# Optimization experiments

Measured on AMD Instinct MI355X. Metric: run time of the kernel, lower is better.

The kernel has to match this reference:

```python
import jax, jax.numpy as jnp
import numpy as np

B, L, D, H = 4, 1024, 1024, 16
HS = D // H
BLOCK = 1024
EPS = 1e-5


def setup_inputs() -> dict:
    key = jax.random.key(0)
    ks = jax.random.split(key, 12)
    s = 0.02
    return {
        "x": jax.random.normal(ks[0], (B, L, D), jnp.float32),
        "ln1_w": jnp.ones((D,), jnp.float32),
        "ln1_b": jnp.zeros((D,), jnp.float32),
        "Wqkv": jax.random.normal(ks[1], (D, 3 * D), jnp.float32) * s,
        "bqkv": jnp.zeros((3 * D,), jnp.float32),
        "Wproj": jax.random.normal(ks[2], (D, D), jnp.float32) * s,
        "bproj": jnp.zeros((D,), jnp.float32),
        "Er": jax.random.normal(ks[3], (BLOCK, HS), jnp.float32) * s,
        "ln2_w": jnp.ones((D,), jnp.float32),
        "ln2_b": jnp.zeros((D,), jnp.float32),
        "Wfc": jax.random.normal(ks[4], (D, 4 * D), jnp.float32) * s,
        "bfc": jnp.zeros((4 * D,), jnp.float32),
        "Wfc2": jax.random.normal(ks[5], (4 * D, D), jnp.float32) * s,
        "bfc2": jnp.zeros((D,), jnp.float32),
    }


def _layernorm(x, w, b):
    mu = jnp.mean(x, axis=-1, keepdims=True)
    var = jnp.mean(jnp.square(x - mu), axis=-1, keepdims=True)
    return (x - mu) * jax.lax.rsqrt(var + EPS) * w + b


def _skew(QEr):
    # Music-Transformer skew: pad one zero column on the left of last dim,
    # reshape (B,H,L,L+1) -> (B,H,L+1,L), drop first row.
    b, h, l, _ = QEr.shape
    padded = jnp.pad(QEr, ((0, 0), (0, 0), (0, 0), (1, 0)))
    return padded.reshape(b, h, l + 1, l)[:, :, 1:, :]


def _block(x, ln1_w, ln1_b, Wqkv, bqkv, Wproj, bproj, Er,
           ln2_w, ln2_b, Wfc, bfc, Wfc2, bfc2):
    b, l, d = x.shape
    # --- attention on ln_1(x) ---
    h = _layernorm(x, ln1_w, ln1_b)
    qkv = h @ Wqkv + bqkv                      # (B, L, 3D)
    q, k, v = jnp.split(qkv, 3, axis=-1)
    q = q.reshape(b, l, H, HS).transpose(0, 2, 1, 3)  # (B,H,L,hs)
    k = k.reshape(b, l, H, HS).transpose(0, 2, 1, 3)
    v = v.reshape(b, l, H, HS).transpose(0, 2, 1, 3)

    start = BLOCK - l
    Er_t = Er[start:, :].T                     # (hs, L)
    QEr = jnp.einsum('bhld,dm->bhlm', q, Er_t)  # (B,H,L,L)
    Srel = _skew(QEr)

    QKt = jnp.einsum('bhld,bhmd->bhlm', q, k)  # (B,H,L,L)
    scale = 1.0 / jnp.sqrt(jnp.asarray(HS, x.dtype))
    att = (QKt + Srel) * scale
    causal = jnp.tril(jnp.ones((l, l), bool))
    att = jnp.where(causal, att, jnp.asarray(-jnp.inf, att.dtype))
    att = jax.nn.softmax(att, axis=-1)
    y = jnp.einsum('bhlm,bhmd->bhld', att, v)  # (B,H,L,hs)
    y = y.transpose(0, 2, 1, 3).reshape(b, l, d)
    a = y @ Wproj + bproj

    x = x + a
    # --- MLP on ln_2(x) ---
    h2 = _layernorm(x, ln2_w, ln2_b)
    m = jax.nn.gelu(h2 @ Wfc + bfc, approximate=False) @ Wfc2 + bfc2
    return x + m


def reference(x, ln1_w, ln1_b, Wqkv, bqkv, Wproj, bproj, Er,
              ln2_w, ln2_b, Wfc, bfc, Wfc2, bfc2):
    return _block(x, ln1_w, ln1_b, Wqkv, bqkv, Wproj, bproj, Er,
                  ln2_w, ln2_b, Wfc, bfc, Wfc2, bfc2)
```

## Files before the change

kernel.cpp:

```cpp
#include <hip/hip_runtime.h>
#include <hip/hip_bf16.h>
#include <math.h>

typedef __attribute__((ext_vector_type(8))) __bf16 bf16x8;
typedef __attribute__((ext_vector_type(4))) float f32x4;

#define LL 1024
#define DD 1024
#define HH 16

#define GLOAD16(g, l)                                              \
  __builtin_amdgcn_global_load_lds(                                \
      (const __attribute__((address_space(1))) void*)(g),          \
      (__attribute__((address_space(3))) void*)(l), 16, 0, 0)

#define FENCE asm volatile("" ::: "memory")
#define BARRIER do { FENCE; __builtin_amdgcn_s_barrier(); FENCE; } while (0)
#define SCHEDB __builtin_amdgcn_sched_barrier(0)

__global__ __launch_bounds__(256) void transpose_cvt(const float* __restrict__ W,
                                                     __hip_bfloat16* __restrict__ Wt,
                                                     int R, int C) {
  __shared__ float tile[32][33];
  int tx = threadIdx.x;
  int r0 = blockIdx.y * 32, c0 = blockIdx.x * 32;
  int r = tx >> 3, c4 = (tx & 7) * 4;
  float4 v = *(const float4*)&W[(size_t)(r0 + r) * C + c0 + c4];
  tile[r][c4 + 0] = v.x; tile[r][c4 + 1] = v.y;
  tile[r][c4 + 2] = v.z; tile[r][c4 + 3] = v.w;
  __syncthreads();
  int c = tx >> 3, r4 = (tx & 7) * 4;
  __hip_bfloat16 o[4];
#pragma unroll
  for (int j = 0; j < 4; ++j) o[j] = __float2bfloat16(tile[r4 + j][c]);
  *(uint2*)&Wt[(size_t)(c0 + c) * R + r0 + r4] = *(const uint2*)o;
}

__global__ __launch_bounds__(256) void cvt_er(const float* __restrict__ Er,
                                              __hip_bfloat16* __restrict__ Erb) {
  int i = blockIdx.x * 256 + threadIdx.x;
  float4 v = *(const float4*)&Er[(size_t)i * 4];
  __hip_bfloat16 o[4];
  o[0] = __float2bfloat16(v.x); o[1] = __float2bfloat16(v.y);
  o[2] = __float2bfloat16(v.z); o[3] = __float2bfloat16(v.w);
  *(uint2*)&Erb[(size_t)i * 4] = *(const uint2*)o;
}

__global__ __launch_bounds__(256) void ln_kernel(const float* __restrict__ X,
                                                 const float* __restrict__ w,
                                                 const float* __restrict__ b,
                                                 __hip_bfloat16* __restrict__ out) {
  int row = blockIdx.x;
  int tid = threadIdx.x;
  const float* xr = X + (size_t)row * DD;
  float4 v = *(const float4*)&xr[tid * 4];
  float s = v.x + v.y + v.z + v.w;
  float s2 = v.x * v.x + v.y * v.y + v.z * v.z + v.w * v.w;
#pragma unroll
  for (int m = 1; m < 64; m <<= 1) {
    s += __shfl_xor(s, m);
    s2 += __shfl_xor(s2, m);
  }
  __shared__ float ps[4], ps2[4];
  int wv_ = tid >> 6, lane = tid & 63;
  if (lane == 0) { ps[wv_] = s; ps2[wv_] = s2; }
  __syncthreads();
  float ts = ps[0] + ps[1] + ps[2] + ps[3];
  float ts2 = ps2[0] + ps2[1] + ps2[2] + ps2[3];
  float mu = ts * (1.0f / DD);
  float var = ts2 * (1.0f / DD) - mu * mu;
  float rs = rsqrtf(var + 1e-5f);
  float4 wv = *(const float4*)&w[tid * 4];
  float4 bv = *(const float4*)&b[tid * 4];
  __hip_bfloat16 o[4];
  o[0] = __float2bfloat16((v.x - mu) * rs * wv.x + bv.x);
  o[1] = __float2bfloat16((v.y - mu) * rs * wv.y + bv.y);
  o[2] = __float2bfloat16((v.z - mu) * rs * wv.z + bv.z);
  o[3] = __float2bfloat16((v.w - mu) * rs * wv.w + bv.w);
  *(uint2*)&out[(size_t)row * DD + tid * 4] = *(const uint2*)o;
}

template <int EPI>
__global__ __launch_bounds__(512, 4) void gemm256x128(const __hip_bfloat16* __restrict__ A,
                                                      const __hip_bfloat16* __restrict__ Bt,
                                                      const float* __restrict__ bias,
                                                      const float* __restrict__ resid,
                                                      void* __restrict__ Cout,
                                                      int M, int N, int K) {
  __shared__ __hip_bfloat16 Ab[3][256][32];
  __shared__ __hip_bfloat16 Bb[3][128][32];
  const int tid = threadIdx.x, lane = tid & 63, w = tid >> 6;
  const int wm = w >> 1, wn = w & 1;

  int nbx = gridDim.x, nwg = nbx * gridDim.y;
  int orig = blockIdx.y * nbx + blockIdx.x;
  int cpx = nwg >> 3;
  int wgid = (orig & 7) * cpx + (orig >> 3);
  int bm0 = (wgid / nbx) * 256, bn0 = (wgid % nbx) * 128;

  const int fr = lane & 15, kq = lane >> 4;
  const int sg = ((lane & 3) ^ ((lane >> 3) & 3)) * 8;
  const int srw = lane >> 2;

  auto stageA = [&](int c, int g, int k0) {
    int u = w * 2 + g;
    const __hip_bfloat16* src = A + (size_t)(bm0 + u * 16 + srw) * K + k0 + sg;
    GLOAD16(src, (char*)Ab + c * 16384 + u * 1024);
  };
  auto stageB = [&](int c, int k0) {
    const __hip_bfloat16* src = Bt + (size_t)(bn0 + w * 16 + srw) * K + k0 + sg;
    GLOAD16(src, (char*)Bb + c * 8192 + w * 1024);
  };
  const int swz = ((kq ^ ((fr >> 1) & 3)) << 4);
  auto ldA = [&](int c, int r) -> bf16x8 {
    return *(const bf16x8*)((const char*)Ab + c * 16384 + r * 64 + swz);
  };
  auto ldB = [&](int c, int r) -> bf16x8 {
    return *(const bf16x8*)((const char*)Bb + c * 8192 + r * 64 + swz);
  };

  f32x4 acc[4][4] = {};
  bf16x8 a[4], b[4];

  const int nt = K >> 5;
#pragma unroll
  for (int tt = 0; tt < 2; ++tt) {
    stageA(tt, 0, tt * 32); stageA(tt, 1, tt * 32); stageB(tt, tt * 32);
  }
  asm volatile("s_waitcnt vmcnt(3)" ::: "memory");
  BARRIER;

  int cur = 0, nxt = 2;
  for (int t = 0; t < nt; ++t) {
#pragma unroll
    for (int mf = 0; mf < 4; ++mf) a[mf] = ldA(cur, wm * 64 + mf * 16 + fr);
#pragma unroll
    for (int nf = 0; nf < 4; ++nf) b[nf] = ldB(cur, wn * 64 + nf * 16 + fr);
    if (t + 2 < nt) {
      stageA(nxt, 0, (t + 2) * 32); stageA(nxt, 1, (t + 2) * 32); stageB(nxt, (t + 2) * 32);
    }
    __builtin_amdgcn_s_setprio(1);
#pragma unroll
    for (int mf = 0; mf < 4; ++mf)
#pragma unroll
      for (int nf = 0; nf < 4; ++nf)
        acc[mf][nf] = __builtin_amdgcn_mfma_f32_16x16x32_bf16(a[mf], b[nf], acc[mf][nf], 0, 0, 0);
    __builtin_amdgcn_s_setprio(0);
    if (t <= nt - 3)      { asm volatile("s_waitcnt vmcnt(3)" ::: "memory"); }
    else if (t == nt - 2) { asm volatile("s_waitcnt vmcnt(0)" ::: "memory"); }
    BARRIER;
    cur = (cur == 2) ? 0 : cur + 1;
    nxt = (nxt == 2) ? 0 : nxt + 1;
  }

#pragma unroll
  for (int nf = 0; nf < 4; ++nf) {
    int col = bn0 + wn * 64 + nf * 16 + fr;
    float bsv = bias[col];
#pragma unroll
    for (int mf = 0; mf < 4; ++mf) {
      int rowb = bm0 + wm * 64 + mf * 16 + kq * 4;
#pragma unroll
      for (int j = 0; j < 4; ++j) {
        int row = rowb + j;
        float v = acc[mf][nf][j] + bsv;
        if (EPI == 1) v = 0.5f * v * (1.0f + erff(v * 0.7071067811865476f));
        if (EPI == 2) {
          ((float*)Cout)[(size_t)row * N + col] = v + resid[(size_t)row * N + col];
        } else {
          ((__hip_bfloat16*)Cout)[(size_t)row * N + col] = __float2bfloat16(v);
        }
      }
    }
  }
}

template <int EPI>
__global__ __launch_bounds__(256) void gemm128p(const __hip_bfloat16* __restrict__ A,
                                                const __hip_bfloat16* __restrict__ Bt,
                                                const float* __restrict__ bias,
                                                const float* __restrict__ resid,
                                                void* __restrict__ Cout,
                                                int M, int N, int K) {
  __shared__ __hip_bfloat16 Ab[5][128][32];
  __shared__ __hip_bfloat16 Bb[5][128][32];
  const int tid = threadIdx.x, lane = tid & 63, w = tid >> 6;
  const int wm = w >> 1, wn = w & 1;

  int nbx = gridDim.x, nwg = nbx * gridDim.y;
  int orig = blockIdx.y * nbx + blockIdx.x;
  int cpx = nwg >> 3;
  int wgid = (orig & 7) * cpx + (orig >> 3);
  int bm0 = (wgid / nbx) * 128, bn0 = (wgid % nbx) * 128;

  const int fr = lane & 15, kq = lane >> 4;
  const int sg = ((lane & 3) ^ ((lane >> 3) & 3)) * 8;
  const int srw = lane >> 2;

  auto stageA = [&](int c, int half, int k0) {
    const __hip_bfloat16* src =
        A + (size_t)(bm0 + half * 64 + w * 16 + srw) * K + k0 + sg;
    GLOAD16(src, (char*)Ab + c * 8192 + half * 4096 + w * 1024);
  };
  auto stageB = [&](int c, int half, int k0) {
    const __hip_bfloat16* src =
        Bt + (size_t)(bn0 + half * 64 + w * 16 + srw) * K + k0 + sg;
    GLOAD16(src, (char*)Bb + c * 8192 + half * 4096 + w * 1024);
  };
  const int swz = ((kq ^ ((fr >> 1) & 3)) << 4);
  auto ldA = [&](int c, int r) -> bf16x8 {
    return *(const bf16x8*)((const char*)Ab + c * 8192 + r * 64 + swz);
  };
  auto ldB = [&](int c, int r) -> bf16x8 {
    return *(const bf16x8*)((const char*)Bb + c * 8192 + r * 64 + swz);
  };

  f32x4 acc[4][4] = {};
  bf16x8 a[4], b[4];

  const int nt = K >> 5;
#pragma unroll
  for (int tt = 0; tt < 4; ++tt) {
    stageA(tt, 0, tt * 32); stageA(tt, 1, tt * 32);
    stageB(tt, 0, tt * 32); stageB(tt, 1, tt * 32);
  }
  asm volatile("s_waitcnt vmcnt(12)" ::: "memory");
  BARRIER;

  int cur = 0, nxt = 4;
  for (int t = 0; t < nt; ++t) {
    const int kn = (t + 4) * 32;
    const bool st = (t + 4 < nt);
#pragma unroll
    for (int mf = 0; mf < 4; ++mf) a[mf] = ldA(cur, wm * 64 + mf * 16 + fr);
#pragma unroll
    for (int nf = 0; nf < 4; ++nf) b[nf] = ldB(cur, wn * 64 + nf * 16 + fr);
    if (st) {
      stageA(nxt, 0, kn); stageA(nxt, 1, kn);
      stageB(nxt, 0, kn); stageB(nxt, 1, kn);
    }
    BARRIER; SCHEDB;
    __builtin_amdgcn_s_setprio(1);
#pragma unroll
    for (int mf = 0; mf < 4; ++mf)
#pragma unroll
      for (int nf = 0; nf < 4; ++nf)
        acc[mf][nf] = __builtin_amdgcn_mfma_f32_16x16x32_bf16(a[mf], b[nf], acc[mf][nf], 0, 0, 0);
    __builtin_amdgcn_s_setprio(0);
    SCHEDB;
    if (t <= nt - 5)      { asm volatile("s_waitcnt vmcnt(12)" ::: "memory"); }
    else if (t == nt - 4) { asm volatile("s_waitcnt vmcnt(8)" ::: "memory"); }
    else if (t == nt - 3) { asm volatile("s_waitcnt vmcnt(4)" ::: "memory"); }
    else if (t == nt - 2) { asm volatile("s_waitcnt vmcnt(0)" ::: "memory"); }
    BARRIER;
    cur = (cur == 4) ? 0 : cur + 1;
    nxt = (nxt == 4) ? 0 : nxt + 1;
  }

#pragma unroll
  for (int nf = 0; nf < 4; ++nf) {
    int col = bn0 + wn * 64 + nf * 16 + fr;
    float bsv = bias[col];
#pragma unroll
    for (int mf = 0; mf < 4; ++mf) {
      int rowb = bm0 + wm * 64 + mf * 16 + kq * 4;
#pragma unroll
      for (int j = 0; j < 4; ++j) {
        int row = rowb + j;
        float v = acc[mf][nf][j] + bsv;
        if (EPI == 1) v = 0.5f * v * (1.0f + erff(v * 0.7071067811865476f));
        if (EPI == 2) {
          ((float*)Cout)[(size_t)row * N + col] = v + resid[(size_t)row * N + col];
        } else {
          ((__hip_bfloat16*)Cout)[(size_t)row * N + col] = __float2bfloat16(v);
        }
      }
    }
  }
}

__global__ __launch_bounds__(256) void attn_mfma(const __hip_bfloat16* __restrict__ qkv,
                                                 const __hip_bfloat16* __restrict__ Erb,
                                                 __hip_bfloat16* __restrict__ Y) {
  __shared__ __hip_bfloat16 k_s[64][72];
  __shared__ __hip_bfloat16 er_s[128][72];
  __shared__ __hip_bfloat16 p_s[4][16][72];
  __shared__ __hip_bfloat16 g_s[4][16][128];
  __shared__ __hip_bfloat16 vt_s[64 * 64];

  int bid = blockIdx.x;
  int qi = 15 - (bid >> 6);
  int head = bid & 63;
  int h = head & 15, b = head >> 4;
  int l0 = qi * 64;
  int tid = threadIdx.x, lane = tid & 63, w = tid >> 6;
  const int fr = lane & 15, kq = lane >> 4;

  const __hip_bfloat16* base = qkv + (size_t)b * (LL * 3072) + h * 64;

  bf16x8 qf[2];
  {
    const __hip_bfloat16* q0 = base + (size_t)(l0 + 16 * w + fr) * 3072 + kq * 8;
    qf[0] = *(const bf16x8*)q0;
    qf[1] = *(const bf16x8*)(q0 + 32);
  }

  const int ksr = tid >> 2, ksd = (tid & 3) * 16;
  const __hip_bfloat16* ksrc = base + 1024 + (size_t)ksr * 3072 + ksd;
  const int vc = (tid >> 3) * 2, vd0 = (tid & 7) * 8;
  const __hip_bfloat16* vsrc = base + 2048 + (size_t)vc * 3072 + vd0;
  const int e0r = tid >> 1, e0c = (tid & 1) * 32;
  const int err = tid >> 2, erc = (tid & 3) * 16;

  uint4 kst0, kst1, vst0, vst1;
  uint4 est0, est1, est2, est3;
  uint4 ers0, ers1;

  {
    kst0 = *(const uint4*)ksrc; kst1 = *(const uint4*)(ksrc + 8);
    vst0 = *(const uint4*)vsrc; vst1 = *(const uint4*)(vsrc + 3072);
    int m = min(max(960 - l0 + e0r, 0), 1023);
    const __hip_bfloat16* ep = Erb + (size_t)m * 64 + e0c;
    est0 = *(const uint4*)ep;        est1 = *(const uint4*)(ep + 8);
    est2 = *(const uint4*)(ep + 16); est3 = *(const uint4*)(ep + 24);
  }

  f32x4 oacc[4] = {};
  float m_run[4], s_run[4];
#pragma unroll
  for (int j = 0; j < 4; ++j) { m_run[j] = -1e30f; s_run[j] = 0.f; }

  auto gchunk = [&](int hf) {
#pragma unroll
    for (int g = 0; g < 4; ++g) {
      int cc = hf * 64 + 16 * g + fr, kc = kq * 8;
      bf16x8 e0 = *(const bf16x8*)&er_s[cc][kc];
      bf16x8 e1 = *(const bf16x8*)&er_s[cc][kc + 32];
      f32x4 gacc = {};
      gacc = __builtin_amdgcn_mfma_f32_16x16x32_bf16(qf[0], e0, gacc, 0, 0, 0);
      gacc = __builtin_amdgcn_mfma_f32_16x16x32_bf16(qf[1], e1, gacc, 0, 0, 0);
#pragma unroll
      for (int j = 0; j < 4; ++j)
        g_s[w][kq * 4 + j][hf * 64 + 16 * g + fr] = __float2bfloat16(gacc[j]);
    }
  };

  for (int t = 0; t <= qi; ++t) {
    __syncthreads();
    *(uint4*)&k_s[ksr][ksd] = kst0;
    *(uint4*)&k_s[ksr][ksd + 8] = kst1;
    {
      const uint16_t* h0 = (const uint16_t*)&vst0;
      const uint16_t* h1 = (const uint16_t*)&vst1;
#pragma unroll
      for (int j = 0; j < 8; ++j) {
        int d = vd0 + j;
        uint32_t pk = (uint32_t)h0[j] | ((uint32_t)h1[j] << 16);
        uint32_t byte = ((uint32_t)d << 7) + 2u * (uint32_t)vc;
        byte ^= (uint32_t)(((d & 7) ^ (d >> 3)) << 4);
        *(uint32_t*)((char*)vt_s + byte) = pk;
      }
    }
    if (t == 0) {
      *(uint4*)&er_s[e0r][e0c]      = est0;
      *(uint4*)&er_s[e0r][e0c + 8]  = est1;
      *(uint4*)&er_s[e0r][e0c + 16] = est2;
      *(uint4*)&er_s[e0r][e0c + 24] = est3;
    } else if (t < qi) {
      int hf = (t + 1) & 1;
      *(uint4*)&er_s[hf * 64 + err][erc]     = ers0;
      *(uint4*)&er_s[hf * 64 + err][erc + 8] = ers1;
    }
    __syncthreads();
    if (t < qi) {
      int c0n = (t + 1) * 64;
      const __hip_bfloat16* kp = ksrc + (size_t)c0n * 3072;
      kst0 = *(const uint4*)kp; kst1 = *(const uint4*)(kp + 8);
      const __hip_bfloat16* vp = vsrc + (size_t)c0n * 3072;
      vst0 = *(const uint4*)vp; vst1 = *(const uint4*)(vp + 3072);
      if (t + 1 < qi) {
        int m = min(960 - l0 + (t + 2) * 64 + err, 1023);
        const __hip_bfloat16* ep = Erb + (size_t)m * 64 + erc;
        ers0 = *(const uint4*)ep; ers1 = *(const uint4*)(ep + 8);
      }
    }
    SCHEDB;

    f32x4 sacc[4] = {};
#pragma unroll
    for (int f = 0; f < 4; ++f) {
      int cc = 16 * f + fr, kc = kq * 8;
      bf16x8 k0 = *(const bf16x8*)&k_s[cc][kc];
      bf16x8 k1 = *(const bf16x8*)&k_s[cc][kc + 32];
      sacc[f] = __builtin_amdgcn_mfma_f32_16x16x32_bf16(qf[0], k0, sacc[f], 0, 0, 0);
      sacc[f] = __builtin_amdgcn_mfma_f32_16x16x32_bf16(qf[1], k1, sacc[f], 0, 0, 0);
    }
    if (t == 0) {
      gchunk(0);
      if (qi > 0) gchunk(1);
    } else if (t < qi) {
      gchunk((t + 1) & 1);
    }

    float sv[4][4];
#pragma unroll
    for (int f = 0; f < 4; ++f) {
#pragma unroll
      for (int j = 0; j < 4; ++j) {
        int r = kq * 4 + j;
        int c = 16 * f + fr;
        int jj = c - (16 * w + r) + 63;
        float g = __bfloat162float(g_s[w][r][(t * 64 + jj) & 127]);
        float val = (sacc[f][j] + g) * 0.125f;
        if (t == qi && c > 16 * w + r) val = -1e30f;
        sv[f][j] = val;
      }
    }
    float alpha[4];
#pragma unroll
    for (int j = 0; j < 4; ++j) {
      float tm = fmaxf(fmaxf(sv[0][j], sv[1][j]), fmaxf(sv[2][j], sv[3][j]));
      tm = fmaxf(tm, __shfl_xor(tm, 1));
      tm = fmaxf(tm, __shfl_xor(tm, 2));
      tm = fmaxf(tm, __shfl_xor(tm, 4));
      tm = fmaxf(tm, __shfl_xor(tm, 8));
      float nm = fmaxf(m_run[j], tm);
      alpha[j] = __expf(m_run[j] - nm);
      m_run[j] = nm;
    }
#pragma unroll
    for (int f = 0; f < 4; ++f)
#pragma unroll
      for (int j = 0; j < 4; ++j)
        sv[f][j] = __expf(sv[f][j] - m_run[j]);
#pragma unroll
    for (int j = 0; j < 4; ++j) {
      float ps = sv[0][j] + sv[1][j] + sv[2][j] + sv[3][j];
      ps += __shfl_xor(ps, 1); ps += __shfl_xor(ps, 2);
      ps += __shfl_xor(ps, 4); ps += __shfl_xor(ps, 8);
      s_run[j] = s_run[j] * alpha[j] + ps;
    }
#pragma unroll
    for (int f = 0; f < 4; ++f)
#pragma unroll
      for (int j = 0; j < 4; ++j)
        oacc[f][j] *= alpha[j];
#pragma unroll
    for (int f = 0; f < 4; ++f)
#pragma unroll
      for (int j = 0; j < 4; ++j)
        p_s[w][kq * 4 + j][16 * f + fr] = __float2bfloat16(sv[f][j]);
#pragma unroll
    for (int kk = 0; kk < 2; ++kk) {
      bf16x8 pf = *(const bf16x8*)&p_s[w][fr][kq * 8 + 32 * kk];
#pragma unroll
      for (int f = 0; f < 4; ++f) {
        int d = 16 * f + fr;
        int cc = kq * 8 + 32 * kk;
        uint32_t byte = ((uint32_t)d << 7) + 2u * (uint32_t)cc;
        byte ^= (uint32_t)(((d & 7) ^ (d >> 3)) << 4);
        bf16x8 vf = *(const bf16x8*)((char*)vt_s + byte);
        oacc[f] = __builtin_amdgcn_mfma_f32_16x16x32_bf16(pf, vf, oacc[f], 0, 0, 0);
      }
    }
  }

#pragma unroll
  for (int f = 0; f < 4; ++f)
#pragma unroll
    for (int j = 0; j < 4; ++j) {
      int r = 16 * w + kq * 4 + j;
      int d = 16 * f + fr;
      float o = oacc[f][j] / s_run[j];
      Y[(size_t)(b * LL + l0 + r) * DD + h * 64 + d] = __float2bfloat16(o);
    }
}

extern "C" void kernel_launch(void* const* d_in, const int* in_sizes, int n_in,
                              void* d_out, int out_size, void* d_ws, size_t ws_size,
                              hipStream_t stream) {
  (void)in_sizes; (void)n_in; (void)out_size; (void)ws_size;
  const float* x     = (const float*)d_in[0];
  const float* ln1w  = (const float*)d_in[1];
  const float* ln1b  = (const float*)d_in[2];
  const float* Wqkv  = (const float*)d_in[3];
  const float* bqkv  = (const float*)d_in[4];
  const float* Wproj = (const float*)d_in[5];
  const float* bproj = (const float*)d_in[6];
  const float* Er    = (const float*)d_in[7];
  const float* ln2w  = (const float*)d_in[8];
  const float* ln2b  = (const float*)d_in[9];
  const float* Wfc   = (const float*)d_in[10];
  const float* bfc   = (const float*)d_in[11];
  const float* Wfc2  = (const float*)d_in[12];
  const float* bfc2  = (const float*)d_in[13];
  float* out = (float*)d_out;

  char* ws = (char*)d_ws;
  const size_t MB = 1ull << 20;
  __hip_bfloat16* h1    = (__hip_bfloat16*)(ws + 0);
  __hip_bfloat16* qkvb  = (__hip_bfloat16*)(ws + 8 * MB);
  __hip_bfloat16* mbuf  = (__hip_bfloat16*)(ws + 0);
  __hip_bfloat16* yb    = (__hip_bfloat16*)(ws + 32 * MB);
  __hip_bfloat16* h2    = (__hip_bfloat16*)(ws + 32 * MB);
  float*          x2    = (float*)(ws + 40 * MB);
  __hip_bfloat16* Wqkvt = (__hip_bfloat16*)(ws + 56 * MB);
  __hip_bfloat16* Erb   = (__hip_bfloat16*)(ws + 62 * MB);
  __hip_bfloat16* Wprojt= (__hip_bfloat16*)(ws + 63 * MB);
  __hip_bfloat16* Wfct  = (__hip_bfloat16*)(ws + 66 * MB);
  __hip_bfloat16* Wfc2t = (__hip_bfloat16*)(ws + 75 * MB);

  dim3 blk(256);

  transpose_cvt<<<dim3(3072 / 32, 1024 / 32), blk, 0, stream>>>(Wqkv, Wqkvt, 1024, 3072);
  transpose_cvt<<<dim3(1024 / 32, 1024 / 32), blk, 0, stream>>>(Wproj, Wprojt, 1024, 1024);
  transpose_cvt<<<dim3(4096 / 32, 1024 / 32), blk, 0, stream>>>(Wfc, Wfct, 1024, 4096);
  transpose_cvt<<<dim3(1024 / 32, 4096 / 32), blk, 0, stream>>>(Wfc2, Wfc2t, 4096, 1024);
  cvt_er<<<dim3(64), blk, 0, stream>>>(Er, Erb);

  ln_kernel<<<4096, blk, 0, stream>>>(x, ln1w, ln1b, h1);

  gemm256x128<0><<<dim3(3072 / 128, 4096 / 256), dim3(512), 0, stream>>>(
      h1, Wqkvt, bqkv, nullptr, qkvb, 4096, 3072, 1024);

  attn_mfma<<<dim3(1024), blk, 0, stream>>>(qkvb, Erb, yb);

  gemm128p<2><<<dim3(1024 / 128, 4096 / 128), blk, 0, stream>>>(
      yb, Wprojt, bproj, x, x2, 4096, 1024, 1024);

  ln_kernel<<<4096, blk, 0, stream>>>(x2, ln2w, ln2b, h2);

  gemm256x128<1><<<dim3(4096 / 128, 4096 / 256), dim3(512), 0, stream>>>(
      h2, Wfct, bfc, nullptr, mbuf, 4096, 4096, 1024);

  gemm128p<2><<<dim3(1024 / 128, 4096 / 128), blk, 0, stream>>>(
      mbuf, Wfc2t, bfc2, x2, out, 4096, 1024, 4096);
}
```

Before: 255.9 us.

## Use 128x64 tiles with 3-stage pipeline for N=1024 GEMMs

Replaces the 128x128 five-stage GEMM used for the projection and FC2 layers with a 128x64 tile kernel that has a three-stage LDS pipeline and a launch-bounds occupancy hint of 2. This doubles the workgroup count (512 instead of 256) to fill the 256 CUs better and removes one barrier per k-step. It also pads the attention g_s buffer to reduce LDS bank conflicts. The cost is lower per-tile reuse (more global traffic for A) and a shallower prefetch depth.

```diff
diff --git a/kernel.cpp b/kernel.cpp
--- a/kernel.cpp
+++ b/kernel.cpp
@@ -176,14 +176,14 @@
 }
 
 template <int EPI>
-__global__ __launch_bounds__(256) void gemm128p(const __hip_bfloat16* __restrict__ A,
-                                                const __hip_bfloat16* __restrict__ Bt,
-                                                const float* __restrict__ bias,
-                                                const float* __restrict__ resid,
-                                                void* __restrict__ Cout,
-                                                int M, int N, int K) {
-  __shared__ __hip_bfloat16 Ab[5][128][32];
-  __shared__ __hip_bfloat16 Bb[5][128][32];
+__global__ __launch_bounds__(256, 2) void gemm128x64(const __hip_bfloat16* __restrict__ A,
+                                                     const __hip_bfloat16* __restrict__ Bt,
+                                                     const float* __restrict__ bias,
+                                                     const float* __restrict__ resid,
+                                                     void* __restrict__ Cout,
+                                                     int M, int N, int K) {
+  __shared__ __hip_bfloat16 Ab[3][128][32];
+  __shared__ __hip_bfloat16 Bb[3][64][32];
   const int tid = threadIdx.x, lane = tid & 63, w = tid >> 6;
   const int wm = w >> 1, wn = w & 1;
 
@@ -191,75 +191,66 @@
   int orig = blockIdx.y * nbx + blockIdx.x;
   int cpx = nwg >> 3;
   int wgid = (orig & 7) * cpx + (orig >> 3);
-  int bm0 = (wgid / nbx) * 128, bn0 = (wgid % nbx) * 128;
+  int bm0 = (wgid / nbx) * 128, bn0 = (wgid % nbx) * 64;
 
   const int fr = lane & 15, kq = lane >> 4;
   const int sg = ((lane & 3) ^ ((lane >> 3) & 3)) * 8;
   const int srw = lane >> 2;
 
-  auto stageA = [&](int c, int half, int k0) {
-    const __hip_bfloat16* src =
-        A + (size_t)(bm0 + half * 64 + w * 16 + srw) * K + k0 + sg;
-    GLOAD16(src, (char*)Ab + c * 8192 + half * 4096 + w * 1024);
-  };
-  auto stageB = [&](int c, int half, int k0) {
-    const __hip_bfloat16* src =
-        Bt + (size_t)(bn0 + half * 64 + w * 16 + srw) * K + k0 + sg;
-    GLOAD16(src, (char*)Bb + c * 8192 + half * 4096 + w * 1024);
+  auto stageA = [&](int c, int g, int k0) {
+    int u = w * 2 + g;
+    const __hip_bfloat16* src = A + (size_t)(bm0 + u * 16 + srw) * K + k0 + sg;
+    GLOAD16(src, (char*)Ab + c * 8192 + u * 1024);
+  };
+  auto stageB = [&](int c, int k0) {
+    const __hip_bfloat16* src = Bt + (size_t)(bn0 + w * 16 + srw) * K + k0 + sg;
+    GLOAD16(src, (char*)Bb + c * 4096 + w * 1024);
   };
   const int swz = ((kq ^ ((fr >> 1) & 3)) << 4);
   auto ldA = [&](int c, int r) -> bf16x8 {
     return *(const bf16x8*)((const char*)Ab + c * 8192 + r * 64 + swz);
   };
   auto ldB = [&](int c, int r) -> bf16x8 {
-    return *(const bf16x8*)((const char*)Bb + c * 8192 + r * 64 + swz);
-  };
-
-  f32x4 acc[4][4] = {};
-  bf16x8 a[4], b[4];
+    return *(const bf16x8*)((const char*)Bb + c * 4096 + r * 64 + swz);
+  };
+
+  f32x4 acc[4][2] = {};
+  bf16x8 a[4], b[2];
 
   const int nt = K >> 5;
 #pragma unroll
-  for (int tt = 0; tt < 4; ++tt) {
-    stageA(tt, 0, tt * 32); stageA(tt, 1, tt * 32);
-    stageB(tt, 0, tt * 32); stageB(tt, 1, tt * 32);
-  }
-  asm volatile("s_waitcnt vmcnt(12)" ::: "memory");
+  for (int tt = 0; tt < 2; ++tt) {
+    stageA(tt, 0, tt * 32); stageA(tt, 1, tt * 32); stageB(tt, tt * 32);
+  }
+  asm volatile("s_waitcnt vmcnt(3)" ::: "memory");
   BARRIER;
 
-  int cur = 0, nxt = 4;
+  int cur = 0, nxt = 2;
   for (int t = 0; t < nt; ++t) {
-    const int kn = (t + 4) * 32;
-    const bool st = (t + 4 < nt);
 #pragma unroll
     for (int mf = 0; mf < 4; ++mf) a[mf] = ldA(cur, wm * 64 + mf * 16 + fr);
 #pragma unroll
-    for (int nf = 0; nf < 4; ++nf) b[nf] = ldB(cur, wn * 64 + nf * 16 + fr);
-    if (st) {
-      stageA(nxt, 0, kn); stageA(nxt, 1, kn);
-      stageB(nxt, 0, kn); stageB(nxt, 1, kn);
-    }
-    BARRIER; SCHEDB;
+    for (int nf = 0; nf < 2; ++nf) b[nf] = ldB(cur, wn * 32 + nf * 16 + fr);
+    if (t + 2 < nt) {
+      stageA(nxt, 0, (t + 2) * 32); stageA(nxt, 1, (t + 2) * 32); stageB(nxt, (t + 2) * 32);
+    }
     __builtin_amdgcn_s_setprio(1);
 #pragma unroll
     for (int mf = 0; mf < 4; ++mf)
 #pragma unroll
-      for (int nf = 0; nf < 4; ++nf)
+      for (int nf = 0; nf < 2; ++nf)
         acc[mf][nf] = __builtin_amdgcn_mfma_f32_16x16x32_bf16(a[mf], b[nf], acc[mf][nf], 0, 0, 0);
     __builtin_amdgcn_s_setprio(0);
-    SCHEDB;
-    if (t <= nt - 5)      { asm volatile("s_waitcnt vmcnt(12)" ::: "memory"); }
-    else if (t == nt - 4) { asm volatile("s_waitcnt vmcnt(8)" ::: "memory"); }
-    else if (t == nt - 3) { asm volatile("s_waitcnt vmcnt(4)" ::: "memory"); }
+    if (t <= nt - 3)      { asm volatile("s_waitcnt vmcnt(3)" ::: "memory"); }
     else if (t == nt - 2) { asm volatile("s_waitcnt vmcnt(0)" ::: "memory"); }
     BARRIER;
-    cur = (cur == 4) ? 0 : cur + 1;
-    nxt = (nxt == 4) ? 0 : nxt + 1;
-  }
-
-#pragma unroll
-  for (int nf = 0; nf < 4; ++nf) {
-    int col = bn0 + wn * 64 + nf * 16 + fr;
+    cur = (cur == 2) ? 0 : cur + 1;
+    nxt = (nxt == 2) ? 0 : nxt + 1;
+  }
+
+#pragma unroll
+  for (int nf = 0; nf < 2; ++nf) {
+    int col = bn0 + wn * 32 + nf * 16 + fr;
     float bsv = bias[col];
 #pragma unroll
     for (int mf = 0; mf < 4; ++mf) {
@@ -285,7 +276,7 @@
   __shared__ __hip_bfloat16 k_s[64][72];
   __shared__ __hip_bfloat16 er_s[128][72];
   __shared__ __hip_bfloat16 p_s[4][16][72];
-  __shared__ __hip_bfloat16 g_s[4][16][128];
+  __shared__ __hip_bfloat16 g_s[4][16][132];
   __shared__ __hip_bfloat16 vt_s[64 * 64];
 
   int bid = blockIdx.x;
@@ -525,7 +516,7 @@
 
   attn_mfma<<<dim3(1024), blk, 0, stream>>>(qkvb, Erb, yb);
 
-  gemm128p<2><<<dim3(1024 / 128, 4096 / 128), blk, 0, stream>>>(
+  gemm128x64<2><<<dim3(1024 / 64, 4096 / 128), blk, 0, stream>>>(
       yb, Wprojt, bproj, x, x2, 4096, 1024, 1024);
 
   ln_kernel<<<4096, blk, 0, stream>>>(x2, ln2w, ln2b, h2);
@@ -533,6 +524,6 @@
   gemm256x128<1><<<dim3(4096 / 128, 4096 / 256), dim3(512), 0, stream>>>(
       h2, Wfct, bfc, nullptr, mbuf, 4096, 4096, 1024);
 
-  gemm128p<2><<<dim3(1024 / 128, 4096 / 128), blk, 0, stream>>>(
+  gemm128x64<2><<<dim3(1024 / 64, 4096 / 128), blk, 0, stream>>>(
       mbuf, Wfc2t, bfc2, x2, out, 4096, 1024, 4096);
 }
```

Result: no change. 251.7 us (-1.7%).
